# Kernel optimization log

Measured on AMD Instinct MI355X. Metric: run time of the kernel, lower is better.

The kernel has to match this reference:

```python
import jax, jax.numpy as jnp
import numpy as np

B, N, H = 4096, 64, 256  # batch, num variables (input_dim == output_dim), hidden_dim
EPS = 1e-5  # nn.LayerNorm default eps


def setup_inputs() -> dict:
    key = jax.random.key(0)
    ks = jax.random.split(key, 10)
    s = lambda k, shape: jax.random.normal(k, shape, dtype=jnp.float32) * 0.05
    return {
        "x": jax.random.normal(ks[0], (B, N), dtype=jnp.float32),
        # flattened GRN: GRN(input_dim=N, hidden_dim=H, output_dim=N)
        "f_fc1_w": s(ks[1], (N, H)), "f_fc1_b": jnp.zeros((H,), jnp.float32),
        "f_fc2_w": s(ks[2], (H, N)), "f_fc2_b": jnp.zeros((N,), jnp.float32),
        "f_skip_w": s(ks[3], (N, N)), "f_skip_b": jnp.zeros((N,), jnp.float32),
        "f_gate_w": s(ks[4], (N, N)), "f_gate_b": jnp.zeros((N,), jnp.float32),
        "f_ln_g": jnp.ones((N,), jnp.float32), "f_ln_b": jnp.zeros((N,), jnp.float32),
        # per-variable GRNs: N copies of GRN(input_dim=1, hidden_dim=H, output_dim=H)
        "g_fc1_w": s(ks[5], (N, H)), "g_fc1_b": jnp.zeros((N, H), jnp.float32),
        "g_fc2_w": s(ks[6], (N, H, H)), "g_fc2_b": jnp.zeros((N, H), jnp.float32),
        "g_skip_w": s(ks[7], (N, H)), "g_skip_b": jnp.zeros((N, H), jnp.float32),
        "g_gate_w": s(ks[8], (N, H)), "g_gate_b": jnp.zeros((N, H), jnp.float32),
        "g_ln_g": jnp.ones((N, H), jnp.float32), "g_ln_b": jnp.zeros((N, H), jnp.float32),
    }


def _layer_norm(x, g, b):
    mu = jnp.mean(x, axis=-1, keepdims=True)
    var = jnp.mean(jnp.square(x - mu), axis=-1, keepdims=True)
    return (x - mu) * jax.lax.rsqrt(var + EPS) * g + b


def reference(x,
              f_fc1_w, f_fc1_b, f_fc2_w, f_fc2_b, f_skip_w, f_skip_b,
              f_gate_w, f_gate_b, f_ln_g, f_ln_b,
              g_fc1_w, g_fc1_b, g_fc2_w, g_fc2_b, g_skip_w, g_skip_b,
              g_gate_w, g_gate_b, g_ln_g, g_ln_b):
    # ---- flattened GRN: GRN(N -> H -> N); dropout is identity in eval mode ----
    h = jax.nn.elu(x @ f_fc1_w + f_fc1_b) @ f_fc2_w + f_fc2_b          # [B, N]
    skip = x @ f_skip_w + f_skip_b                                      # [B, N]
    gate = jax.nn.sigmoid(x @ f_gate_w + f_gate_b)                      # [B, N]
    w = _layer_norm(gate * h + (1.0 - gate) * skip, f_ln_g, f_ln_b)     # [B, N]
    sparse_w = jax.nn.softmax(w, axis=-1)                               # [B, N]

    # ---- per-variable GRNs (input_dim=1 -> hidden H), vectorized over the N variables ----
    xe = x[:, :, None]                                                  # [B, N, 1]
    hv = jax.nn.elu(xe * g_fc1_w + g_fc1_b)                             # [B, N, H] (fc1: 1->H)
    hv = jnp.einsum('bnh,nhk->bnk', hv, g_fc2_w) + g_fc2_b              # [B, N, H] (fc2: H->H per var)
    skv = xe * g_skip_w + g_skip_b                                      # [B, N, H] (skip: 1->H)
    gv = jax.nn.sigmoid(xe * g_gate_w + g_gate_b)                       # [B, N, H] (gate: 1->H)
    emb = _layer_norm(gv * hv + (1.0 - gv) * skv, g_ln_g, g_ln_b)       # [B, N, H]

    # softmax-weighted sum over the variable axis
    combined = jnp.sum(sparse_w[:, :, None] * emb, axis=1)              # [B, H]
    return combined, sparse_w[:, :, None]
```

## Files before the change

kernel.cpp:

```cpp
#include <hip/hip_runtime.h>
#include <hip/hip_bf16.h>

typedef __attribute__((ext_vector_type(4))) float f32x4;
typedef __attribute__((ext_vector_type(8))) short s16x8;

#define W2P_BYTES   8388608ull
#define SLAB_FLOATS 1048576ull
#define WS_NEEDED   (W2P_BYTES + 7ull * SLAB_FLOATS * 4ull)

__global__ __launch_bounds__(256) void k0_pack(const float* __restrict__ w2,
                                               ushort* __restrict__ out) {
  __shared__ float tile[32][257];
  const int n = blockIdx.x >> 3, ks = blockIdx.x & 7;
  const float* src = w2 + ((size_t)n * 256 + ks * 32) * 256;
  for (int i = threadIdx.x; i < 8192; i += 256)
    tile[i >> 8][i & 255] = src[i];
  __syncthreads();
#pragma unroll
  for (int q = 0; q < 4; ++q) {
    int chunk = q * 256 + threadIdx.x;
    int ct = chunk >> 6, l = chunk & 63;
    int g = l >> 4, cl = l & 15;
    s16x8 pk;
#pragma unroll
    for (int j = 0; j < 8; ++j) {
      __hip_bfloat16 h = __float2bfloat16(tile[g * 8 + j][ct * 16 + cl]);
      pk[j] = *reinterpret_cast<short*>(&h);
    }
    *reinterpret_cast<s16x8*>(out + ((size_t)(n * 8 + ks) * 1024 + chunk) * 8) = pk;
  }
}

__global__ __launch_bounds__(256) void k1_select(
    const float* __restrict__ x,
    const float* __restrict__ w1, const float* __restrict__ b1,
    const float* __restrict__ w2, const float* __restrict__ b2,
    const float* __restrict__ wsk, const float* __restrict__ bsk,
    const float* __restrict__ wg, const float* __restrict__ bg,
    const float* __restrict__ lng, const float* __restrict__ lnb,
    float* __restrict__ spw) {
  __shared__ float xs[8][64];
  __shared__ float t1[8][256];
  __shared__ float wvv[8][64];
  const int t = threadIdx.x;
  const int b0 = blockIdx.x * 8;
  if (t < 128) {
    const f32x4* xin = reinterpret_cast<const f32x4*>(x + (size_t)b0 * 64);
    reinterpret_cast<f32x4*>(&xs[0][0])[t] = xin[t];
  }
  __syncthreads();
  {
    float acc[8];
    float bias = b1[t];
#pragma unroll
    for (int r = 0; r < 8; ++r) acc[r] = bias;
    for (int n = 0; n < 64; ++n) {
      float w = w1[n * 256 + t];
#pragma unroll
      for (int r = 0; r < 8; ++r) acc[r] = fmaf(xs[r][n], w, acc[r]);
    }
#pragma unroll
    for (int r = 0; r < 8; ++r) {
      float z = acc[r];
      t1[r][t] = fmaxf(z, 0.f) + (__expf(fminf(z, 0.f)) - 1.f);
    }
  }
  __syncthreads();
  {
    const int nn = t & 63, rg = t >> 6;
    float a2[2], as_[2], ag[2];
    float bb2 = b2[nn], bbs = bsk[nn], bbg = bg[nn];
#pragma unroll
    for (int i = 0; i < 2; ++i) { a2[i] = bb2; as_[i] = bbs; ag[i] = bbg; }
    for (int h = 0; h < 256; ++h) {
      float w = w2[h * 64 + nn];
#pragma unroll
      for (int i = 0; i < 2; ++i) a2[i] = fmaf(t1[rg + 4 * i][h], w, a2[i]);
    }
    for (int m = 0; m < 64; ++m) {
      float ws_ = wsk[m * 64 + nn], wg_ = wg[m * 64 + nn];
#pragma unroll
      for (int i = 0; i < 2; ++i) {
        float xv = xs[rg + 4 * i][m];
        as_[i] = fmaf(xv, ws_, as_[i]);
        ag[i]  = fmaf(xv, wg_, ag[i]);
      }
    }
#pragma unroll
    for (int i = 0; i < 2; ++i) {
      float gt = __fdividef(1.f, 1.f + __expf(-ag[i]));
      wvv[rg + 4 * i][nn] = fmaf(gt, a2[i] - as_[i], as_[i]);
    }
  }
  __syncthreads();
  {
    const int lane = t & 63, wid = t >> 6;
    float gl = lng[lane], bl = lnb[lane];
#pragma unroll
    for (int rr = 0; rr < 2; ++rr) {
      int r = wid * 2 + rr;
      float v = wvv[r][lane];
      float s = v;
      for (int m = 1; m < 64; m <<= 1) s += __shfl_xor(s, m);
      float mu = s * (1.f / 64.f);
      float d = v - mu;
      float q = d * d;
      for (int m = 1; m < 64; m <<= 1) q += __shfl_xor(q, m);
      float wn = d * rsqrtf(q * (1.f / 64.f) + 1e-5f) * gl + bl;
      float mx = wn;
      for (int m = 1; m < 64; m <<= 1) mx = fmaxf(mx, __shfl_xor(mx, m));
      float e = __expf(wn - mx);
      float se = e;
      for (int m = 1; m < 64; m <<= 1) se += __shfl_xor(se, m);
      spw[(size_t)(b0 + r) * 64 + lane] = __fdividef(e, se);
    }
  }
}

template <bool ATOMIC>
__global__ __launch_bounds__(512, 4) void k2_main(
    const float* __restrict__ x,
    const ushort* __restrict__ w2p,
    const float* __restrict__ fc1w, const float* __restrict__ fc1b,
    const float* __restrict__ fc2b,
    const float* __restrict__ skw, const float* __restrict__ skb,
    const float* __restrict__ gww, const float* __restrict__ gwb,
    const float* __restrict__ lng, const float* __restrict__ lnb,
    const float* __restrict__ spw,
    float* __restrict__ comb, float* __restrict__ slabs) {
  __shared__ __align__(16) char Ab[16384];
  __shared__ float xs[32][9];
  __shared__ float ss[32][9];
  __shared__ float sums[2][32][2];

  const int bid = blockIdx.x;
  const int nch = bid & 7;
  const int b0  = (bid >> 3) * 32;
  const int t = threadIdx.x;
  const int lane = t & 63;
  const int w = t >> 6;
  const int g = lane >> 4;
  const int cl = lane & 15;
  const int n0 = nch * 8;

  if (t < 256) {
    int r = t >> 3, j = t & 7;
    xs[r][j] = x[(size_t)(b0 + r) * 64 + nch * 8 + j];
    ss[r][j] = spw[(size_t)(b0 + r) * 64 + nch * 8 + j];
  }
  if (t < 64) (&sums[0][0][0])[t] = 0.f;

  f32x4 comb_acc[2][2];
#pragma unroll
  for (int a = 0; a < 2; ++a)
#pragma unroll
    for (int b = 0; b < 2; ++b) comb_acc[a][b] = (f32x4){0.f, 0.f, 0.f, 0.f};

  const s16x8* wf = reinterpret_cast<const s16x8*>(w2p);
#define BFRAG(nn, kk, ct) \
  (wf + (((size_t)((nn) * 8 + (kk)) * 16 + w * 2 + (ct)) * 64 + lane))

  __syncthreads();

  for (int ni = 0; ni < 8; ++ni) {
    const int n = n0 + ni;
    s16x8 bfa[2], bfb[2];
#pragma unroll
    for (int ct = 0; ct < 2; ++ct) {
      bfa[ct] = *BFRAG(n, 0, ct);
      bfb[ct] = *BFRAG(n, 1, ct);
    }

    {
      const int kc = t & 31;
      const int rb = t >> 5;
      const float* w1p = fc1w + n * 256 + kc * 8;
      const float* b1p = fc1b + n * 256 + kc * 8;
      f32x4 wlo = *reinterpret_cast<const f32x4*>(w1p);
      f32x4 whi = *reinterpret_cast<const f32x4*>(w1p + 4);
      f32x4 blo = *reinterpret_cast<const f32x4*>(b1p);
      f32x4 bhi = *reinterpret_cast<const f32x4*>(b1p + 4);
#pragma unroll
      for (int i = 0; i < 2; ++i) {
        int r = rb + 16 * i;
        float xv = xs[r][ni];
        s16x8 pk;
#pragma unroll
        for (int j = 0; j < 4; ++j) {
          float z0 = fmaf(xv, wlo[j], blo[j]);
          float z1 = fmaf(xv, whi[j], bhi[j]);
          float e0 = fmaxf(z0, 0.f) + (__expf(fminf(z0, 0.f)) - 1.f);
          float e1 = fmaxf(z1, 0.f) + (__expf(fminf(z1, 0.f)) - 1.f);
          __hip_bfloat16 h0 = __float2bfloat16(e0);
          __hip_bfloat16 h1 = __float2bfloat16(e1);
          pk[j]     = *reinterpret_cast<short*>(&h0);
          pk[j + 4] = *reinterpret_cast<short*>(&h1);
        }
        *reinterpret_cast<s16x8*>(Ab + r * 512 + ((kc << 4) ^ ((r & 7) << 4))) = pk;
      }
    }
    __syncthreads();

    f32x4 acc[2][2];
#pragma unroll
    for (int a = 0; a < 2; ++a)
#pragma unroll
      for (int b = 0; b < 2; ++b) acc[a][b] = (f32x4){0.f, 0.f, 0.f, 0.f};

#pragma unroll
    for (int ks = 0; ks < 8; ++ks) {
      s16x8* cur = (ks & 1) ? bfb : bfa;
      s16x8 af[2];
#pragma unroll
      for (int rt = 0; rt < 2; ++rt) {
        int row = rt * 16 + cl;
        af[rt] = *reinterpret_cast<const s16x8*>(
            Ab + row * 512 + (((ks * 4 + g) << 4) ^ ((row & 7) << 4)));
      }
#pragma unroll
      for (int ct = 0; ct < 2; ++ct)
#pragma unroll
        for (int rt = 0; rt < 2; ++rt)
          acc[ct][rt] = __builtin_amdgcn_mfma_f32_16x16x32_bf16(
              cur[ct], af[rt], acc[ct][rt], 0, 0, 0);
      if (ks < 6) {
#pragma unroll
        for (int ct = 0; ct < 2; ++ct) cur[ct] = *BFRAG(n, ks + 2, ct);
      }
    }

    const int par = ni & 1;
    {
      float xr[2], rsum[2], rsq[2];
#pragma unroll
      for (int rt = 0; rt < 2; ++rt) {
        xr[rt] = xs[rt * 16 + cl][ni];
        rsum[rt] = 0.f;
        rsq[rt] = 0.f;
      }
#pragma unroll
      for (int ct = 0; ct < 2; ++ct) {
        const int c4 = n * 256 + (w * 2 + ct) * 16 + g * 4;
        f32x4 f2b4 = *reinterpret_cast<const f32x4*>(fc2b + c4);
        f32x4 sw4  = *reinterpret_cast<const f32x4*>(skw + c4);
        f32x4 sb4  = *reinterpret_cast<const f32x4*>(skb + c4);
        f32x4 gw4  = *reinterpret_cast<const f32x4*>(gww + c4);
        f32x4 gb4  = *reinterpret_cast<const f32x4*>(gwb + c4);
#pragma unroll
        for (int rt = 0; rt < 2; ++rt) {
#pragma unroll
          for (int j = 0; j < 4; ++j) {
            float hv = acc[ct][rt][j] + f2b4[j];
            float sk = fmaf(xr[rt], sw4[j], sb4[j]);
            float gv = __fdividef(1.f, 1.f + __expf(-fmaf(xr[rt], gw4[j], gb4[j])));
            float p = fmaf(gv, hv - sk, sk);
            acc[ct][rt][j] = p;
            rsum[rt] += p;
            rsq[rt] = fmaf(p, p, rsq[rt]);
          }
        }
      }
#pragma unroll
      for (int rt = 0; rt < 2; ++rt) {
        rsum[rt] += __shfl_xor(rsum[rt], 16);
        rsum[rt] += __shfl_xor(rsum[rt], 32);
        rsq[rt]  += __shfl_xor(rsq[rt], 16);
        rsq[rt]  += __shfl_xor(rsq[rt], 32);
      }
      if (g == 0) {
#pragma unroll
        for (int rt = 0; rt < 2; ++rt) {
          atomicAdd(&sums[par][rt * 16 + cl][0], rsum[rt]);
          atomicAdd(&sums[par][rt * 16 + cl][1], rsq[rt]);
        }
      }
    }
    if (t < 64) (&sums[par ^ 1][0][0])[t] = 0.f;
    __syncthreads();

    {
      float rsv[2], mrs[2], svv[2];
#pragma unroll
      for (int rt = 0; rt < 2; ++rt) {
        int row = rt * 16 + cl;
        float s0 = sums[par][row][0], s1 = sums[par][row][1];
        float mu = s0 * (1.f / 256.f);
        float rs = rsqrtf(fmaxf(s1 * (1.f / 256.f) - mu * mu, 0.f) + 1e-5f);
        rsv[rt] = rs;
        mrs[rt] = -mu * rs;
        svv[rt] = ss[row][ni];
      }
#pragma unroll
      for (int ct = 0; ct < 2; ++ct) {
        const int c4 = n * 256 + (w * 2 + ct) * 16 + g * 4;
        f32x4 lg4 = *reinterpret_cast<const f32x4*>(lng + c4);
        f32x4 lb4 = *reinterpret_cast<const f32x4*>(lnb + c4);
#pragma unroll
        for (int rt = 0; rt < 2; ++rt) {
#pragma unroll
          for (int j = 0; j < 4; ++j) {
            float tnorm = fmaf(acc[ct][rt][j], rsv[rt], mrs[rt]);
            float emb = fmaf(tnorm, lg4[j], lb4[j]);
            comb_acc[ct][rt][j] = fmaf(svv[rt], emb, comb_acc[ct][rt][j]);
          }
        }
      }
    }
  }
#undef BFRAG

  float* outp;
  if (ATOMIC) outp = comb;
  else outp = (nch == 0) ? comb : slabs + (size_t)(nch - 1) * SLAB_FLOATS;
#pragma unroll
  for (int ct = 0; ct < 2; ++ct)
#pragma unroll
    for (int rt = 0; rt < 2; ++rt) {
      size_t idx = (size_t)(b0 + rt * 16 + cl) * 256 + (w * 2 + ct) * 16 + g * 4;
      if (ATOMIC) {
#pragma unroll
        for (int j = 0; j < 4; ++j)
          atomicAdd(&outp[idx + j], comb_acc[ct][rt][j]);
      } else {
        *reinterpret_cast<f32x4*>(outp + idx) = comb_acc[ct][rt];
      }
    }
}

__global__ __launch_bounds__(256) void k3_reduce(float* __restrict__ comb,
                                                 const float* __restrict__ slabs) {
  size_t i = (size_t)blockIdx.x * 256 + threadIdx.x;
  f32x4 v = reinterpret_cast<const f32x4*>(comb)[i];
#pragma unroll
  for (int s = 0; s < 7; ++s)
    v += reinterpret_cast<const f32x4*>(slabs)[s * (SLAB_FLOATS / 4) + i];
  reinterpret_cast<f32x4*>(comb)[i] = v;
}

extern "C" void kernel_launch(void* const* d_in, const int* in_sizes, int n_in,
                              void* d_out, int out_size, void* d_ws, size_t ws_size,
                              hipStream_t stream) {
  const float* x   = (const float*)d_in[0];
  const float* f1w = (const float*)d_in[1];
  const float* f1b = (const float*)d_in[2];
  const float* f2w = (const float*)d_in[3];
  const float* f2b = (const float*)d_in[4];
  const float* fsw = (const float*)d_in[5];
  const float* fsb = (const float*)d_in[6];
  const float* fgw = (const float*)d_in[7];
  const float* fgb = (const float*)d_in[8];
  const float* flg = (const float*)d_in[9];
  const float* flb = (const float*)d_in[10];
  const float* g1w = (const float*)d_in[11];
  const float* g1b = (const float*)d_in[12];
  const float* g2w = (const float*)d_in[13];
  const float* g2b = (const float*)d_in[14];
  const float* gsw = (const float*)d_in[15];
  const float* gsb = (const float*)d_in[16];
  const float* ggw = (const float*)d_in[17];
  const float* ggb = (const float*)d_in[18];
  const float* glg = (const float*)d_in[19];
  const float* glb = (const float*)d_in[20];

  float* out  = (float*)d_out;
  float* comb = out;
  float* spw  = out + (size_t)4096 * 256;
  ushort* w2p = (ushort*)d_ws;
  float* slabs = (float*)((char*)d_ws + W2P_BYTES);

  k0_pack<<<512, 256, 0, stream>>>(g2w, w2p);
  k1_select<<<512, 256, 0, stream>>>(x, f1w, f1b, f2w, f2b, fsw, fsb,
                                     fgw, fgb, flg, flb, spw);
  if (ws_size >= WS_NEEDED) {
    k2_main<false><<<1024, 512, 0, stream>>>(x, w2p, g1w, g1b, g2b, gsw, gsb,
                                             ggw, ggb, glg, glb, spw, comb, slabs);
    k3_reduce<<<1024, 256, 0, stream>>>(comb, slabs);
  } else {
    hipMemsetAsync(comb, 0, (size_t)4096 * 256 * sizeof(float), stream);
    k2_main<true><<<1024, 512, 0, stream>>>(x, w2p, g1w, g1b, g2b, gsw, gsb,
                                            ggw, ggb, glg, glb, spw, comb, slabs);
  }
}
```

Before: 151.6 us.

## Software-pipeline k2_main with double-buffered A tile and deferred LayerNorm pass

```diff
diff --git a/kernel.cpp b/kernel.cpp
--- a/kernel.cpp
+++ b/kernel.cpp
@@ -128,10 +128,10 @@
     const float* __restrict__ lng, const float* __restrict__ lnb,
     const float* __restrict__ spw,
     float* __restrict__ comb, float* __restrict__ slabs) {
-  __shared__ __align__(16) char Ab[16384];
+  __shared__ __align__(16) char Ab[2][16384];
   __shared__ float xs[32][9];
   __shared__ float ss[32][9];
-  __shared__ float sums[2][32][2];
+  __shared__ float sums[3][32][2];
 
   const int bid = blockIdx.x;
   const int nch = bid & 7;
@@ -148,9 +148,10 @@
     xs[r][j] = x[(size_t)(b0 + r) * 64 + nch * 8 + j];
     ss[r][j] = spw[(size_t)(b0 + r) * 64 + nch * 8 + j];
   }
-  if (t < 64) (&sums[0][0][0])[t] = 0.f;
+  if (t < 192) (&sums[0][0][0])[t] = 0.f;
 
   f32x4 comb_acc[2][2];
+  f32x4 acc[2][2];
 #pragma unroll
   for (int a = 0; a < 2; ++a)
 #pragma unroll
@@ -160,76 +161,114 @@
 #define BFRAG(nn, kk, ct) \
   (wf + (((size_t)((nn) * 8 + (kk)) * 16 + w * 2 + (ct)) * 64 + lane))
 
-  __syncthreads();
-
+  auto AGEN = [&](int nn, char* abuf) {
+    const int kc = t & 31;
+    const int rb = t >> 5;
+    const int nloc = nn - n0;
+    const float* w1p = fc1w + nn * 256 + kc * 8;
+    const float* b1p = fc1b + nn * 256 + kc * 8;
+    f32x4 wlo = *reinterpret_cast<const f32x4*>(w1p);
+    f32x4 whi = *reinterpret_cast<const f32x4*>(w1p + 4);
+    f32x4 blo = *reinterpret_cast<const f32x4*>(b1p);
+    f32x4 bhi = *reinterpret_cast<const f32x4*>(b1p + 4);
+#pragma unroll
+    for (int i = 0; i < 2; ++i) {
+      int r = rb + 16 * i;
+      float xv = xs[r][nloc];
+      s16x8 pk;
+#pragma unroll
+      for (int j = 0; j < 4; ++j) {
+        float z0 = fmaf(xv, wlo[j], blo[j]);
+        float z1 = fmaf(xv, whi[j], bhi[j]);
+        float e0 = fmaxf(z0, 0.f) + (__expf(fminf(z0, 0.f)) - 1.f);
+        float e1 = fmaxf(z1, 0.f) + (__expf(fminf(z1, 0.f)) - 1.f);
+        __hip_bfloat16 h0 = __float2bfloat16(e0);
+        __hip_bfloat16 h1 = __float2bfloat16(e1);
+        pk[j]     = *reinterpret_cast<short*>(&h0);
+        pk[j + 4] = *reinterpret_cast<short*>(&h1);
+      }
+      *reinterpret_cast<s16x8*>(abuf + r * 512 + ((kc << 4) ^ ((r & 7) << 4))) = pk;
+    }
+  };
+
+  auto PASS2 = [&](int pni) {
+    const int pn = n0 + pni;
+    const float* sb = &sums[pni % 3][0][0];
+    float rsv[2], mrs[2], svv[2];
+#pragma unroll
+    for (int rt = 0; rt < 2; ++rt) {
+      int row = rt * 16 + cl;
+      float s0 = sb[row * 2], s1 = sb[row * 2 + 1];
+      float mu = s0 * (1.f / 256.f);
+      float rs = rsqrtf(fmaxf(s1 * (1.f / 256.f) - mu * mu, 0.f) + 1e-5f);
+      rsv[rt] = rs;
+      mrs[rt] = -mu * rs;
+      svv[rt] = ss[row][pni];
+    }
+#pragma unroll
+    for (int ct = 0; ct < 2; ++ct) {
+      const int c4 = pn * 256 + (w * 2 + ct) * 16 + g * 4;
+      f32x4 lg4 = *reinterpret_cast<const f32x4*>(lng + c4);
+      f32x4 lb4 = *reinterpret_cast<const f32x4*>(lnb + c4);
+#pragma unroll
+      for (int rt = 0; rt < 2; ++rt) {
+#pragma unroll
+        for (int j = 0; j < 4; ++j) {
+          float tnorm = fmaf(acc[ct][rt][j], rsv[rt], mrs[rt]);
+          float emb = fmaf(tnorm, lg4[j], lb4[j]);
+          comb_acc[ct][rt][j] = fmaf(svv[rt], emb, comb_acc[ct][rt][j]);
+        }
+      }
+    }
+  };
+
+  __syncthreads();
+
+  s16x8 wbuf[4][2];
+#pragma unroll
+  for (int s = 0; s < 4; ++s) {
+    wbuf[s][0] = *BFRAG(n0, s, 0);
+    wbuf[s][1] = *BFRAG(n0, s, 1);
+  }
+  AGEN(n0, Ab[0]);
+
+#pragma unroll 1
   for (int ni = 0; ni < 8; ++ni) {
     const int n = n0 + ni;
-    s16x8 bfa[2], bfb[2];
-#pragma unroll
-    for (int ct = 0; ct < 2; ++ct) {
-      bfa[ct] = *BFRAG(n, 0, ct);
-      bfb[ct] = *BFRAG(n, 1, ct);
-    }
-
-    {
-      const int kc = t & 31;
-      const int rb = t >> 5;
-      const float* w1p = fc1w + n * 256 + kc * 8;
-      const float* b1p = fc1b + n * 256 + kc * 8;
-      f32x4 wlo = *reinterpret_cast<const f32x4*>(w1p);
-      f32x4 whi = *reinterpret_cast<const f32x4*>(w1p + 4);
-      f32x4 blo = *reinterpret_cast<const f32x4*>(b1p);
-      f32x4 bhi = *reinterpret_cast<const f32x4*>(b1p + 4);
-#pragma unroll
-      for (int i = 0; i < 2; ++i) {
-        int r = rb + 16 * i;
-        float xv = xs[r][ni];
-        s16x8 pk;
-#pragma unroll
-        for (int j = 0; j < 4; ++j) {
-          float z0 = fmaf(xv, wlo[j], blo[j]);
-          float z1 = fmaf(xv, whi[j], bhi[j]);
-          float e0 = fmaxf(z0, 0.f) + (__expf(fminf(z0, 0.f)) - 1.f);
-          float e1 = fmaxf(z1, 0.f) + (__expf(fminf(z1, 0.f)) - 1.f);
-          __hip_bfloat16 h0 = __float2bfloat16(e0);
-          __hip_bfloat16 h1 = __float2bfloat16(e1);
-          pk[j]     = *reinterpret_cast<short*>(&h0);
-          pk[j + 4] = *reinterpret_cast<short*>(&h1);
-        }
-        *reinterpret_cast<s16x8*>(Ab + r * 512 + ((kc << 4) ^ ((r & 7) << 4))) = pk;
-      }
-    }
     __syncthreads();
 
-    f32x4 acc[2][2];
+    if (t < 64) (&sums[(ni + 1) % 3][0][0])[t] = 0.f;
+    if (ni > 0) PASS2(ni - 1);
+
 #pragma unroll
     for (int a = 0; a < 2; ++a)
 #pragma unroll
       for (int b = 0; b < 2; ++b) acc[a][b] = (f32x4){0.f, 0.f, 0.f, 0.f};
 
+    const char* abase = Ab[ni & 1];
 #pragma unroll
     for (int ks = 0; ks < 8; ++ks) {
-      s16x8* cur = (ks & 1) ? bfb : bfa;
       s16x8 af[2];
 #pragma unroll
       for (int rt = 0; rt < 2; ++rt) {
         int row = rt * 16 + cl;
         af[rt] = *reinterpret_cast<const s16x8*>(
-            Ab + row * 512 + (((ks * 4 + g) << 4) ^ ((row & 7) << 4)));
+            abase + row * 512 + (((ks * 4 + g) << 4) ^ ((row & 7) << 4)));
       }
 #pragma unroll
       for (int ct = 0; ct < 2; ++ct)
 #pragma unroll
         for (int rt = 0; rt < 2; ++rt)
           acc[ct][rt] = __builtin_amdgcn_mfma_f32_16x16x32_bf16(
-              cur[ct], af[rt], acc[ct][rt], 0, 0, 0);
-      if (ks < 6) {
-#pragma unroll
-        for (int ct = 0; ct < 2; ++ct) cur[ct] = *BFRAG(n, ks + 2, ct);
-      }
-    }
-
-    const int par = ni & 1;
+              wbuf[ks & 3][ct], af[rt], acc[ct][rt], 0, 0, 0);
+      if (ni < 7 || ks < 4) {
+        const int nn2 = n + ((ks + 4) >> 3);
+        const int kk2 = (ks + 4) & 7;
+        wbuf[ks & 3][0] = *BFRAG(nn2, kk2, 0);
+        wbuf[ks & 3][1] = *BFRAG(nn2, kk2, 1);
+      }
+    }
+
     {
       float xr[2], rsum[2], rsq[2];
 #pragma unroll
@@ -268,45 +307,20 @@
         rsq[rt]  += __shfl_xor(rsq[rt], 32);
       }
       if (g == 0) {
+        float* sb = &sums[ni % 3][0][0];
 #pragma unroll
         for (int rt = 0; rt < 2; ++rt) {
-          atomicAdd(&sums[par][rt * 16 + cl][0], rsum[rt]);
-          atomicAdd(&sums[par][rt * 16 + cl][1], rsq[rt]);
+          atomicAdd(&sb[(rt * 16 + cl) * 2 + 0], rsum[rt]);
+          atomicAdd(&sb[(rt * 16 + cl) * 2 + 1], rsq[rt]);
         }
       }
     }
-    if (t < 64) (&sums[par ^ 1][0][0])[t] = 0.f;
-    __syncthreads();
-
-    {
-      float rsv[2], mrs[2], svv[2];
-#pragma unroll
-      for (int rt = 0; rt < 2; ++rt) {
-        int row = rt * 16 + cl;
-        float s0 = sums[par][row][0], s1 = sums[par][row][1];
-        float mu = s0 * (1.f / 256.f);
-        float rs = rsqrtf(fmaxf(s1 * (1.f / 256.f) - mu * mu, 0.f) + 1e-5f);
-        rsv[rt] = rs;
-        mrs[rt] = -mu * rs;
-        svv[rt] = ss[row][ni];
-      }
-#pragma unroll
-      for (int ct = 0; ct < 2; ++ct) {
-        const int c4 = n * 256 + (w * 2 + ct) * 16 + g * 4;
-        f32x4 lg4 = *reinterpret_cast<const f32x4*>(lng + c4);
-        f32x4 lb4 = *reinterpret_cast<const f32x4*>(lnb + c4);
-#pragma unroll
-        for (int rt = 0; rt < 2; ++rt) {
-#pragma unroll
-          for (int j = 0; j < 4; ++j) {
-            float tnorm = fmaf(acc[ct][rt][j], rsv[rt], mrs[rt]);
-            float emb = fmaf(tnorm, lg4[j], lb4[j]);
-            comb_acc[ct][rt][j] = fmaf(svv[rt], emb, comb_acc[ct][rt][j]);
-          }
-        }
-      }
-    }
-  }
+
+    if (ni < 7) AGEN(n + 1, Ab[(ni + 1) & 1]);
+  }
+
+  __syncthreads();
+  PASS2(7);
 #undef BFRAG
 
   float* outp;
```

Result: slower. 174.6 us (+15.1%).

## Prefetch per-variable epilogue params into double-buffered LDS via async global_load_lds

Applied to the files above, without the earlier changes.

```diff
diff --git a/kernel.cpp b/kernel.cpp
--- a/kernel.cpp
+++ b/kernel.cpp
@@ -129,6 +129,7 @@
     const float* __restrict__ spw,
     float* __restrict__ comb, float* __restrict__ slabs) {
   __shared__ __align__(16) char Ab[16384];
+  __shared__ __align__(16) float pbuf[2][1792];
   __shared__ float xs[32][9];
   __shared__ float ss[32][9];
   __shared__ float sums[2][32][2];
@@ -150,6 +151,25 @@
   }
   if (t < 64) (&sums[0][0][0])[t] = 0.f;
 
+  auto STAGE = [&](int nn, int buf) {
+    if (w < 7) {
+      const float* ps;
+      switch (w) {
+        case 0: ps = fc2b; break;
+        case 1: ps = skw;  break;
+        case 2: ps = skb;  break;
+        case 3: ps = gww;  break;
+        case 4: ps = gwb;  break;
+        case 5: ps = lng;  break;
+        default: ps = lnb; break;
+      }
+      __builtin_amdgcn_global_load_lds(
+          (const __attribute__((address_space(1))) unsigned int*)(ps + nn * 256 + lane * 4),
+          (__attribute__((address_space(3))) unsigned int*)&pbuf[buf][w * 256],
+          16, 0, 0);
+    }
+  };
+
   f32x4 comb_acc[2][2];
 #pragma unroll
   for (int a = 0; a < 2; ++a)
@@ -160,6 +180,7 @@
 #define BFRAG(nn, kk, ct) \
   (wf + (((size_t)((nn) * 8 + (kk)) * 16 + w * 2 + (ct)) * 64 + lane))
 
+  STAGE(n0, 0);
   __syncthreads();
 
   for (int ni = 0; ni < 8; ++ni) {
@@ -201,6 +222,8 @@
     }
     __syncthreads();
 
+    if (ni < 7) STAGE(n + 1, (ni + 1) & 1);
+
     f32x4 acc[2][2];
 #pragma unroll
     for (int a = 0; a < 2; ++a)
@@ -230,6 +253,7 @@
     }
 
     const int par = ni & 1;
+    const float* pb = &pbuf[ni & 1][0];
     {
       float xr[2], rsum[2], rsq[2];
 #pragma unroll
@@ -240,12 +264,12 @@
       }
 #pragma unroll
       for (int ct = 0; ct < 2; ++ct) {
-        const int c4 = n * 256 + (w * 2 + ct) * 16 + g * 4;
-        f32x4 f2b4 = *reinterpret_cast<const f32x4*>(fc2b + c4);
-        f32x4 sw4  = *reinterpret_cast<const f32x4*>(skw + c4);
-        f32x4 sb4  = *reinterpret_cast<const f32x4*>(skb + c4);
-        f32x4 gw4  = *reinterpret_cast<const f32x4*>(gww + c4);
-        f32x4 gb4  = *reinterpret_cast<const f32x4*>(gwb + c4);
+        const int cl4 = (w * 2 + ct) * 16 + g * 4;
+        f32x4 f2b4 = *reinterpret_cast<const f32x4*>(pb + 0 * 256 + cl4);
+        f32x4 sw4  = *reinterpret_cast<const f32x4*>(pb + 1 * 256 + cl4);
+        f32x4 sb4  = *reinterpret_cast<const f32x4*>(pb + 2 * 256 + cl4);
+        f32x4 gw4  = *reinterpret_cast<const f32x4*>(pb + 3 * 256 + cl4);
+        f32x4 gb4  = *reinterpret_cast<const f32x4*>(pb + 4 * 256 + cl4);
 #pragma unroll
         for (int rt = 0; rt < 2; ++rt) {
 #pragma unroll
@@ -292,9 +316,9 @@
       }
 #pragma unroll
       for (int ct = 0; ct < 2; ++ct) {
-        const int c4 = n * 256 + (w * 2 + ct) * 16 + g * 4;
-        f32x4 lg4 = *reinterpret_cast<const f32x4*>(lng + c4);
-        f32x4 lb4 = *reinterpret_cast<const f32x4*>(lnb + c4);
+        const int cl4 = (w * 2 + ct) * 16 + g * 4;
+        f32x4 lg4 = *reinterpret_cast<const f32x4*>(pb + 5 * 256 + cl4);
+        f32x4 lb4 = *reinterpret_cast<const f32x4*>(pb + 6 * 256 + cl4);
 #pragma unroll
         for (int rt = 0; rt < 2; ++rt) {
 #pragma unroll
```

Result: faster. 136.4 us (-10.0%).
